# Kernel tuning notes

Hardware: AMD Instinct MI355X
Metric: run time of the kernel (lower is better)

Reference implementation:

```python
import jax, jax.numpy as jnp
import numpy as np

B, T, C, E = 2, 100, 80, 32
MH = MW = 64
IN_H = IN_W = 640.0
IOU_FACTOR, CLS_FACTOR, TOPK = 6.0, 0.5, 10
EPS = 1e-9


def get_anchors_and_scalers(fmaps, in_h, in_w):
    anchors, scalers = [], []
    for fh, fw in fmaps:
        stride = in_h / fh
        ys = (np.arange(fh) + 0.5) * stride
        xs = (np.arange(fw) + 0.5) * stride
        gy, gx = np.meshgrid(ys, xs, indexing='ij')
        anchors.append(np.stack([gx, gy], -1).reshape(-1, 2))
        scalers.append(np.full(fh * fw, stride))
    return (np.concatenate(anchors).astype(np.float32),
            np.concatenate(scalers).astype(np.float32))


def setup_inputs() -> dict:
    key = jax.random.key(0)
    ks = jax.random.split(key, 8)
    anchors_np, scalers_np = get_anchors_and_scalers([(80, 80), (40, 40), (20, 20)], IN_H, IN_W)
    anchors = jnp.asarray(anchors_np)
    scalers = jnp.asarray(scalers_np)
    A = anchors.shape[0]
    cls_logits = jax.random.normal(ks[0], (B, A, C), jnp.float32)
    wh = jax.random.uniform(ks[1], (B, A, 2), jnp.float32, 16.0, 160.0)
    ctr = anchors[None] + jax.random.normal(ks[2], (B, A, 2), jnp.float32) * 8.0
    pred_boxes = jnp.clip(jnp.concatenate([ctr - wh / 2, ctr + wh / 2], -1), 0.0, IN_W)
    mask_embs = jax.random.normal(ks[3], (B, A, E), jnp.float32)
    protos = jax.random.normal(ks[4], (B, MH, MW, E), jnp.float32)
    tl = jax.random.uniform(ks[5], (B, T, 2), jnp.float32, 0.0, 560.0)
    twh = jax.random.uniform(ks[6], (B, T, 2), jnp.float32, 30.0, 240.0)
    target_bbox = jnp.concatenate([tl, jnp.minimum(tl + twh, IN_W)], -1)
    target_cls = jax.random.randint(ks[7], (B, T), 0, C, jnp.int32)
    target_masks = (jax.random.uniform(jax.random.fold_in(key, 7), (B, MH, MW, T)) > 0.5).astype(jnp.float32)
    return {'cls_logits': cls_logits, 'pred_boxes': pred_boxes, 'mask_embs': mask_embs,
            'protos': protos, 'target_cls': target_cls, 'target_bbox': target_bbox,
            'target_masks': target_masks, 'anchors': anchors, 'scalers': scalers}


def _ciou_pairwise(gt, pr):
    # gt [B,T,4], pr [B,A,4] -> [B,T,A]
    g = gt[:, :, None, :]
    p = pr[:, None, :, :]
    ix1 = jnp.maximum(g[..., 0], p[..., 0]); iy1 = jnp.maximum(g[..., 1], p[..., 1])
    ix2 = jnp.minimum(g[..., 2], p[..., 2]); iy2 = jnp.minimum(g[..., 3], p[..., 3])
    inter = jnp.clip(ix2 - ix1, 0.0) * jnp.clip(iy2 - iy1, 0.0)
    wg = g[..., 2] - g[..., 0]; hg = g[..., 3] - g[..., 1]
    wp = p[..., 2] - p[..., 0]; hp = p[..., 3] - p[..., 1]
    union = wg * hg + wp * hp - inter + EPS
    iou = inter / union
    cw = jnp.maximum(g[..., 2], p[..., 2]) - jnp.minimum(g[..., 0], p[..., 0])
    ch = jnp.maximum(g[..., 3], p[..., 3]) - jnp.minimum(g[..., 1], p[..., 1])
    c2 = cw * cw + ch * ch + EPS
    rho2 = ((g[..., 0] + g[..., 2] - p[..., 0] - p[..., 2]) ** 2 +
            (g[..., 1] + g[..., 3] - p[..., 1] - p[..., 3]) ** 2) / 4.0
    v = (4.0 / (jnp.pi ** 2)) * (jnp.arctan(wg / (hg + EPS)) - jnp.arctan(wp / (hp + EPS))) ** 2
    alpha = jax.lax.stop_gradient(v / (1.0 - iou + v + EPS))
    return iou - rho2 / c2 - alpha * v


def _bbox_mask(boxes, mh, mw, in_h, in_w):
    # boxes [B,A,4] pixel xyxy -> [B,A,mh,mw] binary inside-box mask on mask grid
    sx, sy = mw / in_w, mh / in_h
    x1, y1, x2, y2 = boxes[..., 0] * sx, boxes[..., 1] * sy, boxes[..., 2] * sx, boxes[..., 3] * sy
    rows = jnp.arange(mh, dtype=boxes.dtype)
    cols = jnp.arange(mw, dtype=boxes.dtype)
    rm = (rows >= y1[..., None]) & (rows < y2[..., None])  # [B,A,mh]
    cm = (cols >= x1[..., None]) & (cols < x2[..., None])  # [B,A,mw]
    return (rm[..., :, None] & cm[..., None, :]).astype(boxes.dtype)


def _assign_and_build(cls_logits, pred_boxes, mask_embs, protos,
                      target_cls, target_bbox, target_masks, anchors, scalers):
    Bn, A, Cn = cls_logits.shape
    mh, mw = protos.shape[1], protos.shape[2]
    # --- task-aligned assigner ---
    lt, rb = target_bbox[:, :, None, :2], target_bbox[:, :, None, 2:]
    deltas = jnp.concatenate([anchors[None, None] - lt, rb - anchors[None, None]], -1)
    grid_mask = (jnp.min(deltas, -1) > 0).astype(cls_logits.dtype)  # [B,T,A]
    iou_mat = jnp.clip(_ciou_pairwise(target_bbox, pred_boxes), 0.0, 1.0)  # [B,T,A]
    cls_prob = jax.nn.sigmoid(cls_logits)  # [B,A,C]
    oh_t = jax.nn.one_hot(target_cls, Cn, dtype=cls_prob.dtype)  # [B,T,C]
    cls_mat = jnp.einsum('btc,bac->bta', oh_t, cls_prob)  # [B,T,A]
    tmat = grid_mask * (iou_mat ** IOU_FACTOR) * (cls_mat ** CLS_FACTOR)
    kth = jax.lax.top_k(tmat, TOPK)[0][..., -1:]  # [B,T,1]
    topk_targets = jnp.where((tmat >= kth) & (tmat > 0), tmat, 0.0)
    unique_idx = jnp.argmax(topk_targets, axis=1)  # [B,A] best GT per anchor
    valid = (jnp.sum(topk_targets, axis=1) > 0).astype(cls_logits.dtype)  # [B,A]
    align_bbox = jnp.take_along_axis(target_bbox, jnp.broadcast_to(unique_idx[..., None], (Bn, A, 4)), axis=1)
    align_cls_idx = jnp.take_along_axis(target_cls, unique_idx, axis=1)  # [B,A]
    max_target = jnp.max(tmat, axis=-1, keepdims=True)
    max_iou = jnp.max(iou_mat, axis=-1, keepdims=True)
    norm_term = tmat / (max_target + EPS) * max_iou  # [B,T,A]
    norm_g = jnp.take_along_axis(jnp.transpose(norm_term, (0, 2, 1)), unique_idx[..., None], axis=2)  # [B,A,1]
    align_cls = jax.nn.one_hot(align_cls_idx, Cn, dtype=cls_logits.dtype) * norm_g * valid[..., None]
    # --- loss-target assembly (compute_loss body) ---
    align_bbox_scaled = align_bbox / scalers[None, :, None]
    boxes_scaled = pred_boxes / scalers[None, :, None]
    box_target = jnp.concatenate([align_bbox_scaled, valid[..., None], align_cls], -1)
    box_mask = _bbox_mask(align_bbox, mh, mw, IN_H, IN_W)  # [B,A,mh,mw]
    valid_seg = box_mask * valid[..., None, None]
    seg_pred = jax.nn.sigmoid(jnp.einsum('bne,bhwe->bnhw', mask_embs, protos)) * valid_seg
    seg_pred = seg_pred.reshape(Bn, A, mh * mw)
    masks_t = jnp.transpose(target_masks, (0, 3, 1, 2))  # [B,T,mh,mw]
    idx4 = jnp.broadcast_to(unique_idx[..., None, None], (Bn, A, mh, mw))
    align_seg = (jnp.take_along_axis(masks_t, idx4, axis=1) * valid_seg).reshape(Bn, A, mh * mw)
    area = ((align_bbox[..., 2] - align_bbox[..., 0]) * (align_bbox[..., 3] - align_bbox[..., 1])
            / (IN_W * IN_H))
    seg_target = jnp.concatenate([area[..., None], valid[..., None], align_seg], -1)
    return jnp.concatenate([boxes_scaled, cls_logits, box_target, seg_pred, seg_target], -1)


def reference(cls_logits, pred_boxes, mask_embs, protos, target_cls, target_bbox,
              target_masks, anchors, scalers):
    return _assign_and_build(cls_logits, pred_boxes, mask_embs, protos,
                             target_cls, target_bbox, target_masks, anchors, scalers)
```

## Files before the change

### kernel.cpp

```cpp
#include <hip/hip_runtime.h>
#include <math.h>

#define A_TOT 8400
#define B_N   2
#define T_N   100
#define C_N   80
#define E_N   32
#define MH_N  64
#define MW_N  64
#define ROW_N 8363
#define NROWS (B_N*A_TOT)
#define EPSF  1e-9f
#define NCHUNK 4
#define CHUNK_A 2100
#define COMP_CAP 1280
#define NEGINF -1e30f

typedef float vfloat4 __attribute__((ext_vector_type(4)));

__global__ __launch_bounds__(256) void k_prep(
    const float* __restrict__ pred_boxes, const float* __restrict__ target_bbox,
    float* __restrict__ pred_atan, float* __restrict__ tgt_atan) {
  int i = blockIdx.x * 256 + threadIdx.x;
  if (i < NROWS) {
    float4 pb = *(const float4*)(pred_boxes + (size_t)i*4);
    pred_atan[i] = atanf((pb.z - pb.x) / ((pb.w - pb.y) + EPSF));
  }
  if (i < B_N*T_N) {
    float4 g = *(const float4*)(target_bbox + i*4);
    tgt_atan[i] = atanf((g.z - g.x) / ((g.w - g.y) + EPSF));
  }
}

__device__ __forceinline__ float2 tmat_eval(
    float gx1, float gy1, float gx2, float gy2,
    float ax,  float ay,
    float px1, float py1, float px2, float py2,
    float cl, float atg, float atp) {
  float ix1 = fmaxf(gx1,px1), iy1 = fmaxf(gy1,py1);
  float ix2 = fminf(gx2,px2), iy2 = fminf(gy2,py2);
  float inter = fmaxf(ix2-ix1,0.f) * fmaxf(iy2-iy1,0.f);
  float wg = gx2-gx1, hg = gy2-gy1, wp = px2-px1, hp = py2-py1;
  float uni = wg*hg + wp*hp - inter + EPSF;
  float iou = inter / uni;
  float cw = fmaxf(gx2,px2) - fminf(gx1,px1);
  float ch = fmaxf(gy2,py2) - fminf(gy1,py1);
  float c2 = cw*cw + ch*ch + EPSF;
  float dx = gx1+gx2-px1-px2, dy = gy1+gy2-py1-py2;
  float rho2 = (dx*dx + dy*dy) * 0.25f;
  float da = atg - atp;
  float v  = 0.4052847345693511f * da * da;
  float alpha = v / (1.f - iou + v + EPSF);
  float ciou = iou - rho2/c2 - alpha*v;
  float iouc = fminf(fmaxf(ciou, 0.f), 1.f);

  float tm = 0.f;
  if (ax > gx1 && ay > gy1 && ax < gx2 && ay < gy2) {
    float cp = 1.f / (1.f + expf(-cl));
    float i2 = iouc * iouc;
    tm = i2*i2*i2 * sqrtf(cp);
  }
  return make_float2(tm, iouc);
}

__global__ __launch_bounds__(256) void k_score(
    const float* __restrict__ cls_logits, const float* __restrict__ pred_boxes,
    const float* __restrict__ target_bbox, const int* __restrict__ target_cls,
    const float* __restrict__ anchors,
    const float* __restrict__ pred_atan, const float* __restrict__ tgt_atan,
    float* __restrict__ tmat, float* __restrict__ top10s,
    float* __restrict__ pmaxt, float* __restrict__ pmaxi) {
  int chunk = blockIdx.x;
  int bt    = blockIdx.y;
  int b     = bt / T_N;
  int tid   = threadIdx.x;
  __shared__ float comp[COMP_CAP];
  __shared__ float red[256];
  __shared__ int   cnt, sidx;
  if (tid == 0) cnt = 0;
  __syncthreads();

  float4 g  = *(const float4*)(target_bbox + bt*4);
  int    tc = target_cls[bt];
  float atg = tgt_atan[bt];
  float* trow = tmat + (size_t)bt * A_TOT;

  int a0 = chunk * CHUNK_A;
  float lm = 0.f, li = 0.f;
  for (int a = a0 + tid; a < a0 + CHUNK_A; a += 256) {
    float ax = anchors[a*2+0], ay = anchors[a*2+1];
    float4 pb = *(const float4*)(pred_boxes + ((size_t)(b*A_TOT+a))*4);
    float cl = cls_logits[((size_t)(b*A_TOT+a))*C_N + tc];
    float2 r = tmat_eval(g.x,g.y,g.z,g.w, ax,ay, pb.x,pb.y,pb.z,pb.w,
                         cl, atg, pred_atan[b*A_TOT + a]);
    trow[a] = r.x;
    li = fmaxf(li, r.y);
    if (r.x > 0.f) {
      lm = fmaxf(lm, r.x);
      int i = atomicAdd(&cnt, 1);
      if (i < COMP_CAP) comp[i] = r.x;
    }
  }
  red[tid] = lm; __syncthreads();
  for (int s = 128; s > 0; s >>= 1) { if (tid < s) red[tid] = fmaxf(red[tid], red[tid+s]); __syncthreads(); }
  if (tid == 0) pmaxt[bt*NCHUNK + chunk] = red[0];
  __syncthreads();
  red[tid] = li; __syncthreads();
  for (int s = 128; s > 0; s >>= 1) { if (tid < s) red[tid] = fmaxf(red[tid], red[tid+s]); __syncthreads(); }
  if (tid == 0) pmaxi[bt*NCHUNK + chunk] = red[0];
  __syncthreads();
  int count = min(cnt, COMP_CAP);

  float* t10 = top10s + ((size_t)bt*NCHUNK + chunk) * 10;
  for (int k = 0; k < 10; k++) {
    float l = NEGINF;
    for (int i = tid; i < count; i += 256) l = fmaxf(l, comp[i]);
    red[tid] = l; __syncthreads();
    for (int s = 128; s > 0; s >>= 1) { if (tid < s) red[tid] = fmaxf(red[tid], red[tid+s]); __syncthreads(); }
    float m = red[0];
    if (tid == 0) sidx = 0x7fffffff;
    __syncthreads();
    if (m > NEGINF) {
      for (int i = tid; i < count; i += 256) if (comp[i] == m) atomicMin(&sidx, i);
    }
    __syncthreads();
    if (tid == 0) {
      if (sidx != 0x7fffffff) comp[sidx] = NEGINF;
      t10[k] = m;
    }
    __syncthreads();
  }
}

__global__ __launch_bounds__(64) void k_merge(
    const float* __restrict__ top10s, const float* __restrict__ pmaxt,
    const float* __restrict__ pmaxi,
    float* __restrict__ kth, float* __restrict__ maxt, float* __restrict__ maxiou) {
  int bt = blockIdx.x;
  int lane = threadIdx.x;
  float cand = (lane < NCHUNK*10) ? top10s[(size_t)bt*NCHUNK*10 + lane] : NEGINF;
  float cur = NEGINF;
  #pragma unroll
  for (int k = 0; k < 10; k++) {
    float v = cand; int id = lane;
    #pragma unroll
    for (int off = 32; off; off >>= 1) {
      float ov = __shfl_xor(v, off); int oid = __shfl_xor(id, off);
      if (ov > v || (ov == v && oid < id)) { v = ov; id = oid; }
    }
    if (id == lane) cand = NEGINF;
    cur = v;
  }
  float pm = (lane < NCHUNK) ? pmaxt[bt*NCHUNK + lane] : 0.f;
  float pi = (lane < NCHUNK) ? pmaxi[bt*NCHUNK + lane] : 0.f;
  #pragma unroll
  for (int off = 32; off; off >>= 1) {
    pm = fmaxf(pm, __shfl_xor(pm, off));
    pi = fmaxf(pi, __shfl_xor(pi, off));
  }
  if (lane == 0) {
    kth[bt]    = fmaxf(cur, 0.f);
    maxt[bt]   = pm;
    maxiou[bt] = pi;
  }
}

__global__ __launch_bounds__(256) void k_row(
    const float* __restrict__ cls_logits, const float* __restrict__ pred_boxes,
    const float* __restrict__ mask_embs,  const float* __restrict__ protos,
    const float* __restrict__ t_masks,    const float* __restrict__ tmat,
    const float* __restrict__ kth, const float* __restrict__ maxt,
    const float* __restrict__ maxiou, const float* __restrict__ target_bbox,
    const int* __restrict__ target_cls, const float* __restrict__ scalers,
    float* __restrict__ out) {
  unsigned row = blockIdx.x;
  int b   = row >= (unsigned)A_TOT;
  int a   = (int)row - b*A_TOT;
  int tid = threadIdx.x;
  __shared__ float sv[128];
  __shared__ int   st[128];
  __shared__ float semb[E_N];
  __shared__ float ctx[10];

  if (tid < 128) {
    float v = 0.f; int tt = 0x7fff;
    if (tid < T_N) {
      int bt = b*T_N + tid;
      float tv = tmat[(size_t)bt*A_TOT + a];
      if (tv > 0.f && tv >= kth[bt]) { v = tv; tt = tid; }
    }
    sv[tid] = v; st[tid] = tt;
  }
  if (tid < E_N) semb[tid] = mask_embs[(size_t)row*E_N + tid];
  __syncthreads();
  if (tid < 64) {
    float v1 = sv[tid];    int t1 = st[tid];
    float v2 = sv[tid+64]; int t2 = st[tid+64];
    if (v2 > v1 || (v2 == v1 && t2 < t1)) { v1 = v2; t1 = t2; }
    #pragma unroll
    for (int off = 32; off; off >>= 1) {
      float ov = __shfl_xor(v1, off); int ot = __shfl_xor(t1, off);
      if (ov > v1 || (ov == v1 && ot < t1)) { v1 = ov; t1 = ot; }
    }
    if (tid == 0) {
      int anyv = v1 > 0.f;
      int u = anyv ? t1 : 0;
      int bu = b*T_N + u;
      float4 tb = *(const float4*)(target_bbox + bu*4);
      float ng = anyv ? v1 / (maxt[bu] + EPSF) * maxiou[bu] : 0.f;
      ctx[0]=tb.x; ctx[1]=tb.y; ctx[2]=tb.z; ctx[3]=tb.w;
      ctx[4]= anyv ? 1.f : 0.f; ctx[5]=ng; ctx[6]=scalers[a];
      ctx[7]= (tb.z-tb.x)*(tb.w-tb.y)/(640.f*640.f);
      ctx[8]=__int_as_float(u); ctx[9]=__int_as_float(target_cls[bu]);
    }
  }
  __syncthreads();
  float tb0=ctx[0], tb1=ctx[1], tb2=ctx[2], tb3=ctx[3];
  float vld=ctx[4], ng=ctx[5], s=ctx[6], area=ctx[7];
  int   u  =__float_as_int(ctx[8]), ct=__float_as_int(ctx[9]);
  bool valid = vld > 0.5f;
  float x1s=tb0*0.1f, y1s=tb1*0.1f, x2s=tb2*0.1f, y2s=tb3*0.1f;
  size_t base = (size_t)row * ROW_N;

  auto val = [&](unsigned p) -> float {
    if (p < 84u) {
      if (p < 4u) return pred_boxes[(size_t)row*4 + p] / s;
      return cls_logits[(size_t)row*C_N + (p-4u)];
    }
    if (p < 169u) {
      if (p < 88u) { float t=(p==84u)?tb0:((p==85u)?tb1:((p==86u)?tb2:tb3)); return t/s; }
      if (p == 88u) return vld;
      return (valid && (int)p - 89 == ct) ? ng : 0.f;
    }
    if (p < 4265u) {
      if (!valid) return 0.f;
      unsigned q = p - 169u; int h = q >> 6, w = q & 63;
      float fh = (float)h, fw = (float)w;
      if (!(fh >= y1s && fh < y2s && fw >= x1s && fw < x2s)) return 0.f;
      const float* pr = protos + ((size_t)((b*MH_N + h)*MW_N + w)) * E_N;
      float acc = 0.f;
      #pragma unroll
      for (int e = 0; e < E_N; e++) acc += semb[e] * pr[e];
      return 1.f / (1.f + expf(-acc));
    }
    if (p == 4265u) return area;
    if (p == 4266u) return vld;
    if (!valid) return 0.f;
    unsigned q = p - 4267u; int h = q >> 6, w = q & 63;
    float fh = (float)h, fw = (float)w;
    if (!(fh >= y1s && fh < y2s && fw >= x1s && fw < x2s)) return 0.f;
    return t_masks[((size_t)((b*MH_N + h)*MW_N + w)) * T_N + u];
  };

  unsigned head = (4u - ((row * (unsigned)ROW_N) & 3u)) & 3u;
  if (tid < (int)head) out[base + tid] = val(tid);
  unsigned vec_end = head + (((unsigned)ROW_N - head) & ~3u);
  for (unsigned p = head + 4u*(unsigned)tid; p < vec_end; p += 1024u) {
    vfloat4 o;
    bool pure = (p >= 4267u) || (p >= 169u && p + 4u <= 4265u);
    if (pure && !valid) {
      o = (vfloat4)(0.f);
    } else {
      o.x = val(p); o.y = val(p+1u); o.z = val(p+2u); o.w = val(p+3u);
    }
    __builtin_nontemporal_store(o, (vfloat4*)(out + base + p));
  }
  unsigned tail_n = (unsigned)ROW_N - vec_end;
  if (tid >= 32 && tid < 32 + (int)tail_n)
    out[base + vec_end + (unsigned)(tid - 32)] = val(vec_end + (unsigned)(tid - 32));
}

extern "C" void kernel_launch(void* const* d_in, const int* in_sizes, int n_in,
                              void* d_out, int out_size, void* d_ws, size_t ws_size,
                              hipStream_t stream) {
  const float* cls_logits   = (const float*)d_in[0];
  const float* pred_boxes   = (const float*)d_in[1];
  const float* mask_embs    = (const float*)d_in[2];
  const float* protos       = (const float*)d_in[3];
  const int*   target_cls   = (const int*)  d_in[4];
  const float* target_bbox  = (const float*)d_in[5];
  const float* target_masks = (const float*)d_in[6];
  const float* anchors      = (const float*)d_in[7];
  const float* scalers      = (const float*)d_in[8];
  float* out = (float*)d_out;

  float* ws        = (float*)d_ws;
  float* tmat      = ws;
  float* pred_atan = tmat + (size_t)B_N*T_N*A_TOT;
  float* tgt_atan  = pred_atan + NROWS;
  float* top10s    = tgt_atan + B_N*T_N;
  float* pmaxt     = top10s + (size_t)B_N*T_N*NCHUNK*10;
  float* pmaxi     = pmaxt + B_N*T_N*NCHUNK;
  float* kth       = pmaxi + B_N*T_N*NCHUNK;
  float* maxt      = kth + B_N*T_N;
  float* maxiou    = maxt + B_N*T_N;

  k_prep<<<(NROWS + 255)/256, 256, 0, stream>>>(pred_boxes, target_bbox,
                                                pred_atan, tgt_atan);
  dim3 gS(NCHUNK, B_N*T_N);
  k_score<<<gS, 256, 0, stream>>>(cls_logits, pred_boxes, target_bbox,
                                  target_cls, anchors, pred_atan, tgt_atan,
                                  tmat, top10s, pmaxt, pmaxi);
  k_merge<<<B_N*T_N, 64, 0, stream>>>(top10s, pmaxt, pmaxi, kth, maxt, maxiou);
  k_row<<<NROWS, 256, 0, stream>>>(cls_logits, pred_boxes, mask_embs, protos,
                                   target_masks, tmat, kth, maxt, maxiou,
                                   target_bbox, target_cls, scalers, out);
}
```

Before: 189.5 us.

## Fuse atan prep, scoring and top-k merge into one per-target kernel

Drops the separate atan precompute and merge kernels. One 512-thread block per (batch, target) now computes the CIoU and alignment scores over all anchors, with the atan terms computed inline. Per-block maxima and the 10th-largest score are found with wave shuffles plus a small shared-memory merge, replacing the repeated block-wide reductions. This removes two launches and the intermediate global buffers, but cuts the scoring grid from 800 to 200 blocks and repeats the per-anchor atan for every target. The compaction buffer no longer has a bounds check, so more than 1536 positive anchors for one target would write out of bounds.

```diff
diff --git a/kernel.cpp b/kernel.cpp
--- a/kernel.cpp
+++ b/kernel.cpp
@@ -11,26 +11,10 @@
 #define ROW_N 8363
 #define NROWS (B_N*A_TOT)
 #define EPSF  1e-9f
-#define NCHUNK 4
-#define CHUNK_A 2100
-#define COMP_CAP 1280
+#define COMP_CAP 1536
 #define NEGINF -1e30f
 
 typedef float vfloat4 __attribute__((ext_vector_type(4)));
-
-__global__ __launch_bounds__(256) void k_prep(
-    const float* __restrict__ pred_boxes, const float* __restrict__ target_bbox,
-    float* __restrict__ pred_atan, float* __restrict__ tgt_atan) {
-  int i = blockIdx.x * 256 + threadIdx.x;
-  if (i < NROWS) {
-    float4 pb = *(const float4*)(pred_boxes + (size_t)i*4);
-    pred_atan[i] = atanf((pb.z - pb.x) / ((pb.w - pb.y) + EPSF));
-  }
-  if (i < B_N*T_N) {
-    float4 g = *(const float4*)(target_bbox + i*4);
-    tgt_atan[i] = atanf((g.z - g.x) / ((g.w - g.y) + EPSF));
-  }
-}
 
 __device__ __forceinline__ float2 tmat_eval(
     float gx1, float gy1, float gx2, float gy2,
@@ -63,105 +47,102 @@
   return make_float2(tm, iouc);
 }
 
-__global__ __launch_bounds__(256) void k_score(
+__global__ __launch_bounds__(512) void k_score(
     const float* __restrict__ cls_logits, const float* __restrict__ pred_boxes,
     const float* __restrict__ target_bbox, const int* __restrict__ target_cls,
     const float* __restrict__ anchors,
-    const float* __restrict__ pred_atan, const float* __restrict__ tgt_atan,
-    float* __restrict__ tmat, float* __restrict__ top10s,
-    float* __restrict__ pmaxt, float* __restrict__ pmaxi) {
-  int chunk = blockIdx.x;
-  int bt    = blockIdx.y;
-  int b     = bt / T_N;
-  int tid   = threadIdx.x;
+    float* __restrict__ tmat,
+    float* __restrict__ kth, float* __restrict__ maxt, float* __restrict__ maxiou) {
+  int bt   = blockIdx.x;
+  int b    = bt / T_N;
+  int tid  = threadIdx.x;
+  int lane = tid & 63, wid = tid >> 6;
   __shared__ float comp[COMP_CAP];
-  __shared__ float red[256];
-  __shared__ int   cnt, sidx;
+  __shared__ float redm[8], redi[8];
+  __shared__ float wtop[8][10];
+  __shared__ int   cnt;
   if (tid == 0) cnt = 0;
   __syncthreads();
 
   float4 g  = *(const float4*)(target_bbox + bt*4);
   int    tc = target_cls[bt];
-  float atg = tgt_atan[bt];
+  float atg = atanf((g.z - g.x) / ((g.w - g.y) + EPSF));
   float* trow = tmat + (size_t)bt * A_TOT;
 
-  int a0 = chunk * CHUNK_A;
   float lm = 0.f, li = 0.f;
-  for (int a = a0 + tid; a < a0 + CHUNK_A; a += 256) {
+  for (int a = tid; a < A_TOT; a += 512) {
     float ax = anchors[a*2+0], ay = anchors[a*2+1];
     float4 pb = *(const float4*)(pred_boxes + ((size_t)(b*A_TOT+a))*4);
     float cl = cls_logits[((size_t)(b*A_TOT+a))*C_N + tc];
+    float atp = atanf((pb.z - pb.x) / ((pb.w - pb.y) + EPSF));
     float2 r = tmat_eval(g.x,g.y,g.z,g.w, ax,ay, pb.x,pb.y,pb.z,pb.w,
-                         cl, atg, pred_atan[b*A_TOT + a]);
+                         cl, atg, atp);
     trow[a] = r.x;
     li = fmaxf(li, r.y);
     if (r.x > 0.f) {
       lm = fmaxf(lm, r.x);
-      int i = atomicAdd(&cnt, 1);
-      if (i < COMP_CAP) comp[i] = r.x;
-    }
-  }
-  red[tid] = lm; __syncthreads();
-  for (int s = 128; s > 0; s >>= 1) { if (tid < s) red[tid] = fmaxf(red[tid], red[tid+s]); __syncthreads(); }
-  if (tid == 0) pmaxt[bt*NCHUNK + chunk] = red[0];
-  __syncthreads();
-  red[tid] = li; __syncthreads();
-  for (int s = 128; s > 0; s >>= 1) { if (tid < s) red[tid] = fmaxf(red[tid], red[tid+s]); __syncthreads(); }
-  if (tid == 0) pmaxi[bt*NCHUNK + chunk] = red[0];
-  __syncthreads();
-  int count = min(cnt, COMP_CAP);
-
-  float* t10 = top10s + ((size_t)bt*NCHUNK + chunk) * 10;
-  for (int k = 0; k < 10; k++) {
-    float l = NEGINF;
-    for (int i = tid; i < count; i += 256) l = fmaxf(l, comp[i]);
-    red[tid] = l; __syncthreads();
-    for (int s = 128; s > 0; s >>= 1) { if (tid < s) red[tid] = fmaxf(red[tid], red[tid+s]); __syncthreads(); }
-    float m = red[0];
-    if (tid == 0) sidx = 0x7fffffff;
-    __syncthreads();
-    if (m > NEGINF) {
-      for (int i = tid; i < count; i += 256) if (comp[i] == m) atomicMin(&sidx, i);
-    }
-    __syncthreads();
-    if (tid == 0) {
-      if (sidx != 0x7fffffff) comp[sidx] = NEGINF;
-      t10[k] = m;
-    }
-    __syncthreads();
-  }
-}
-
-__global__ __launch_bounds__(64) void k_merge(
-    const float* __restrict__ top10s, const float* __restrict__ pmaxt,
-    const float* __restrict__ pmaxi,
-    float* __restrict__ kth, float* __restrict__ maxt, float* __restrict__ maxiou) {
-  int bt = blockIdx.x;
-  int lane = threadIdx.x;
-  float cand = (lane < NCHUNK*10) ? top10s[(size_t)bt*NCHUNK*10 + lane] : NEGINF;
-  float cur = NEGINF;
+      comp[atomicAdd(&cnt, 1)] = r.x;
+    }
+  }
+  #pragma unroll
+  for (int off = 32; off; off >>= 1) {
+    lm = fmaxf(lm, __shfl_xor(lm, off));
+    li = fmaxf(li, __shfl_xor(li, off));
+  }
+  if (lane == 0) { redm[wid] = lm; redi[wid] = li; }
+  __syncthreads();
+  if (tid == 0) {
+    float m = redm[0], mi = redi[0];
+    #pragma unroll
+    for (int w = 1; w < 8; w++) { m = fmaxf(m, redm[w]); mi = fmaxf(mi, redi[w]); }
+    maxt[bt] = m; maxiou[bt] = mi;
+  }
+  int count = cnt;
+
+  int base = wid*64 + lane;
+  float e0 = (base        < count) ? comp[base]        : NEGINF;
+  float e1 = (base + 512  < count) ? comp[base + 512]  : NEGINF;
+  float e2 = (base + 1024 < count) ? comp[base + 1024] : NEGINF;
+  float mytop = NEGINF;
   #pragma unroll
   for (int k = 0; k < 10; k++) {
-    float v = cand; int id = lane;
+    float bv = e0; int bs = 0;
+    if (e1 > bv) { bv = e1; bs = 1; }
+    if (e2 > bv) { bv = e2; bs = 2; }
+    float v = bv; int id = (lane << 2) | bs;
     #pragma unroll
     for (int off = 32; off; off >>= 1) {
       float ov = __shfl_xor(v, off); int oid = __shfl_xor(id, off);
       if (ov > v || (ov == v && oid < id)) { v = ov; id = oid; }
     }
-    if (id == lane) cand = NEGINF;
-    cur = v;
-  }
-  float pm = (lane < NCHUNK) ? pmaxt[bt*NCHUNK + lane] : 0.f;
-  float pi = (lane < NCHUNK) ? pmaxi[bt*NCHUNK + lane] : 0.f;
-  #pragma unroll
-  for (int off = 32; off; off >>= 1) {
-    pm = fmaxf(pm, __shfl_xor(pm, off));
-    pi = fmaxf(pi, __shfl_xor(pi, off));
-  }
-  if (lane == 0) {
-    kth[bt]    = fmaxf(cur, 0.f);
-    maxt[bt]   = pm;
-    maxiou[bt] = pi;
+    if ((id >> 2) == lane) {
+      int s = id & 3;
+      if (s == 0) e0 = NEGINF; else if (s == 1) e1 = NEGINF; else e2 = NEGINF;
+    }
+    if (lane == k) mytop = v;
+  }
+  if (lane < 10) wtop[wid][lane] = mytop;
+  __syncthreads();
+
+  if (wid == 0) {
+    int ia = lane, ib = 64 + lane;
+    float f0 = wtop[ia/10][ia%10];
+    float f1 = (ib < 80) ? wtop[ib/10][ib%10] : NEGINF;
+    float cur = NEGINF;
+    #pragma unroll
+    for (int k = 0; k < 10; k++) {
+      float bv = f0; int bs = 0;
+      if (f1 > bv) { bv = f1; bs = 1; }
+      float v = bv; int id = (lane << 1) | bs;
+      #pragma unroll
+      for (int off = 32; off; off >>= 1) {
+        float ov = __shfl_xor(v, off); int oid = __shfl_xor(id, off);
+        if (ov > v || (ov == v && oid < id)) { v = ov; id = oid; }
+      }
+      if ((id >> 1) == lane) { if ((id & 1) == 0) f0 = NEGINF; else f1 = NEGINF; }
+      cur = v;
+    }
+    if (lane == 0) kth[bt] = fmaxf(cur, 0.f);
   }
 }
 
@@ -284,24 +265,14 @@
   const float* scalers      = (const float*)d_in[8];
   float* out = (float*)d_out;
 
-  float* ws        = (float*)d_ws;
-  float* tmat      = ws;
-  float* pred_atan = tmat + (size_t)B_N*T_N*A_TOT;
-  float* tgt_atan  = pred_atan + NROWS;
-  float* top10s    = tgt_atan + B_N*T_N;
-  float* pmaxt     = top10s + (size_t)B_N*T_N*NCHUNK*10;
-  float* pmaxi     = pmaxt + B_N*T_N*NCHUNK;
-  float* kth       = pmaxi + B_N*T_N*NCHUNK;
-  float* maxt      = kth + B_N*T_N;
-  float* maxiou    = maxt + B_N*T_N;
-
-  k_prep<<<(NROWS + 255)/256, 256, 0, stream>>>(pred_boxes, target_bbox,
-                                                pred_atan, tgt_atan);
-  dim3 gS(NCHUNK, B_N*T_N);
-  k_score<<<gS, 256, 0, stream>>>(cls_logits, pred_boxes, target_bbox,
-                                  target_cls, anchors, pred_atan, tgt_atan,
-                                  tmat, top10s, pmaxt, pmaxi);
-  k_merge<<<B_N*T_N, 64, 0, stream>>>(top10s, pmaxt, pmaxi, kth, maxt, maxiou);
+  float* ws     = (float*)d_ws;
+  float* tmat   = ws;
+  float* kth    = tmat + (size_t)B_N*T_N*A_TOT;
+  float* maxt   = kth + B_N*T_N;
+  float* maxiou = maxt + B_N*T_N;
+
+  k_score<<<B_N*T_N, 512, 0, stream>>>(cls_logits, pred_boxes, target_bbox,
+                                       target_cls, anchors, tmat, kth, maxt, maxiou);
   k_row<<<NROWS, 256, 0, stream>>>(cls_logits, pred_boxes, mask_embs, protos,
                                    target_masks, tmat, kth, maxt, maxiou,
                                    target_bbox, target_cls, scalers, out);
```

After: 180.7 us. 4.6% less time.
